# Performance work log

Hardware: AMD Instinct MI355X
Metric: run time of the kernel (lower is better)

## Reference

```python
import jax, jax.numpy as jnp
import numpy as np

EMBED_DIM = 384
NUM_HEADS = 6
HEAD_DIM = EMBED_DIM // NUM_HEADS
MLP_HIDDEN = 4 * EMBED_DIM
LN_EPS = 1e-5


def layer_norm(x, gamma, beta):
    mu = jnp.mean(x, axis=-1, keepdims=True)
    var = jnp.mean((x - mu) ** 2, axis=-1, keepdims=True)
    return (x - mu) * jax.lax.rsqrt(var + LN_EPS) * gamma + beta


def setup_inputs() -> dict:
    key = jax.random.key(0)
    ks = jax.random.split(key, 8)
    D, H = EMBED_DIM, MLP_HIDDEN
    s = 1.0 / np.sqrt(D)
    sh = 1.0 / np.sqrt(H)
    return {
        "x": jax.random.normal(ks[0], (16, 1024, D), dtype=jnp.float32),
        "ln1_g": jnp.ones((D,), jnp.float32),
        "ln1_b": jnp.zeros((D,), jnp.float32),
        "qkv_w": jax.random.uniform(ks[1], (3 * D, D), jnp.float32, -s, s),
        "qkv_b": jax.random.uniform(ks[2], (3 * D,), jnp.float32, -s, s),
        "proj_w": jax.random.uniform(ks[3], (D, D), jnp.float32, -s, s),
        "proj_b": jax.random.uniform(ks[4], (D,), jnp.float32, -s, s),
        "ln2_g": jnp.ones((D,), jnp.float32),
        "ln2_b": jnp.zeros((D,), jnp.float32),
        "fc1_w": jax.random.uniform(ks[5], (H, D), jnp.float32, -s, s),
        "fc1_b": jax.random.uniform(ks[6], (H,), jnp.float32, -s, s),
        "fc2_w": jax.random.uniform(ks[7], (D, H), jnp.float32, -sh, sh),
        "fc2_b": jnp.zeros((D,), jnp.float32),
    }


def reference(x, ln1_g, ln1_b, qkv_w, qkv_b, proj_w, proj_b,
              ln2_g, ln2_b, fc1_w, fc1_b, fc2_w, fc2_b):
    B, N, D = x.shape
    Hh, Dh = NUM_HEADS, HEAD_DIM
    scale = Dh ** -0.5

    # --- attention sublayer (pre-norm) ---
    h = layer_norm(x, ln1_g, ln1_b)
    qkv = h @ qkv_w.T + qkv_b                      # [B,N,3D]
    qkv = qkv.reshape(B, N, 3, Hh, Dh)
    q, k, v = (qkv[:, :, i].transpose(0, 2, 1, 3) for i in range(3))  # [B,H,N,Dh]
    attn = jax.nn.softmax(jnp.einsum('bhnd,bhmd->bhnm', q, k) * scale, axis=-1)
    o = jnp.einsum('bhnm,bhmd->bhnd', attn, v)     # [B,H,N,Dh]
    o = o.transpose(0, 2, 1, 3).reshape(B, N, D)
    x = x + (o @ proj_w.T + proj_b)

    # --- MLP sublayer (pre-norm) ---
    h = layer_norm(x, ln2_g, ln2_b)
    h = jax.nn.gelu(h @ fc1_w.T + fc1_b, approximate=False)
    x = x + (h @ fc2_w.T + fc2_b)
    return x
```

## Files before the change

### kernel.cpp

```cpp
#include <hip/hip_runtime.h>

typedef unsigned short u16;
typedef unsigned int   u32;
typedef __bf16  bf16x8 __attribute__((ext_vector_type(8)));
typedef __bf16  bf16x4_t __attribute__((ext_vector_type(4)));
typedef float   f32x4  __attribute__((ext_vector_type(4)));
typedef float   f32x2  __attribute__((ext_vector_type(2)));

struct Ptrs { const void* p[13]; };

extern "C" __device__ float __ocml_native_exp2_f32(float);

__device__ __forceinline__ float bf2f(u16 u) {
    union { unsigned int i; float f; } c; c.i = ((unsigned int)u) << 16; return c.f;
}
__device__ __forceinline__ u16 f2bf(float f) {
    union { float f; unsigned int i; } c; c.f = f;
    unsigned int u = c.i;
    unsigned int r = (u + 0x7fffu + ((u >> 16) & 1u)) >> 16;
    return (u16)r;
}

__device__ __forceinline__ float wave_sum(float x) {
#pragma unroll
    for (int m = 32; m >= 1; m >>= 1) x += __shfl_xor(x, m);
    return x;
}

__device__ __forceinline__ void g2l16(const u16* g, u16* l) {
    __builtin_amdgcn_global_load_lds(
        (__attribute__((address_space(1))) void*)g,
        (__attribute__((address_space(3))) void*)l, 16, 0, 0);
}

__device__ __forceinline__ int sniff_bf16(const u32* __restrict__ w) {
    int cnt = 0;
    for (int i = 0; i < 128; ++i) {
        u16 lo = (u16)(w[i] & 0xFFFFu);
        int e = (lo >> 7) & 0xFF;
        cnt += (e >= 117 && e <= 123) ? 1 : 0;
    }
    return (cnt >= 64) ? 1 : 0;
}

__global__ __launch_bounds__(256) void k_convert(Ptrs ps,
                                                 u16* __restrict__ cw,
                                                 int* __restrict__ flagp)
{
    const int cum[13] = {0,48,96,55392,55536,73968,74016,74064,74112,
                         147840,148032,221760,221808};
    const int off[12] = {0,384,768,443136,444288,591744,
                         592128,592512,592896,1182720,1184256,1774080};
    const int flag = sniff_bf16((const u32*)ps.p[3]);
    if (blockIdx.x == 0 && threadIdx.x == 0) *flagp = flag;
    int c = blockIdx.x * 256 + threadIdx.x;
    if (c >= 221808) return;
    int seg = 0;
#pragma unroll
    for (int i = 1; i < 12; ++i) seg += (c >= cum[i]) ? 1 : 0;
    int e = (c - cum[seg]) * 8;
    u16* dst = cw + off[seg] + e;
    if (flag) {
        *(uint4*)dst = *((const uint4*)ps.p[seg + 1] + (e >> 3));
    } else {
        const float* s = (const float*)ps.p[seg + 1] + e;
        u16 tmp[8];
#pragma unroll
        for (int t = 0; t < 8; ++t) tmp[t] = f2bf(s[t]);
        *(uint4*)dst = *(const uint4*)tmp;
    }
}

__global__ __launch_bounds__(256) void k_ln1cvt(const void* __restrict__ xin,
                                                const u16* __restrict__ g,
                                                const u16* __restrict__ b,
                                                u16* __restrict__ cx,
                                                u16* __restrict__ h,
                                                const int* __restrict__ flagp)
{
    const int wid = threadIdx.x >> 6, lane = threadIdx.x & 63;
    const int row = blockIdx.x * 4 + wid;
    const int e0 = lane * 6;
    float v[6]; u16 raw[6];
    if (*flagp) {
        const u16* p = (const u16*)xin + (size_t)row * 384 + e0;
        u32 w0 = *(const u32*)(p);
        u32 w1 = *(const u32*)(p + 2);
        u32 w2 = *(const u32*)(p + 4);
        raw[0] = (u16)w0; raw[1] = (u16)(w0 >> 16);
        raw[2] = (u16)w1; raw[3] = (u16)(w1 >> 16);
        raw[4] = (u16)w2; raw[5] = (u16)(w2 >> 16);
#pragma unroll
        for (int t = 0; t < 6; t++) v[t] = bf2f(raw[t]);
    } else {
        const float* p = (const float*)xin + (size_t)row * 384 + e0;
        f32x2 a0 = *(const f32x2*)(p);
        f32x2 a1 = *(const f32x2*)(p + 2);
        f32x2 a2 = *(const f32x2*)(p + 4);
        v[0] = a0[0]; v[1] = a0[1]; v[2] = a1[0];
        v[3] = a1[1]; v[4] = a2[0]; v[5] = a2[1];
#pragma unroll
        for (int t = 0; t < 6; t++) raw[t] = f2bf(v[t]);
    }
    u32* pc = (u32*)(cx + (size_t)row * 384 + e0);
    pc[0] = (u32)raw[0] | ((u32)raw[1] << 16);
    pc[1] = (u32)raw[2] | ((u32)raw[3] << 16);
    pc[2] = (u32)raw[4] | ((u32)raw[5] << 16);
    float s = 0.f;
#pragma unroll
    for (int t = 0; t < 6; t++) s += v[t];
    const float mu = wave_sum(s) * (1.0f / 384.0f);
    float vs = 0.f;
#pragma unroll
    for (int t = 0; t < 6; t++) { float d = v[t] - mu; vs += d * d; }
    const float var = wave_sum(vs) * (1.0f / 384.0f);
    const float rs = rsqrtf(var + 1e-5f);
    const u32* gg = (const u32*)(g + e0);
    const u32* bb = (const u32*)(b + e0);
    u32 gw[3] = {gg[0], gg[1], gg[2]};
    u32 bw[3] = {bb[0], bb[1], bb[2]};
    u16 ow[6];
#pragma unroll
    for (int t = 0; t < 6; t++) {
        u16 ge = (u16)(gw[t >> 1] >> ((t & 1) * 16));
        u16 be = (u16)(bw[t >> 1] >> ((t & 1) * 16));
        ow[t] = f2bf((v[t] - mu) * rs * bf2f(ge) + bf2f(be));
    }
    u32* po = (u32*)(h + (size_t)row * 384 + e0);
    po[0] = (u32)ow[0] | ((u32)ow[1] << 16);
    po[1] = (u32)ow[2] | ((u32)ow[3] << 16);
    po[2] = (u32)ow[4] | ((u32)ow[5] << 16);
}

__device__ __forceinline__ void gemm_core_128(const u16* __restrict__ A,
                                              const u16* __restrict__ B,
                                              int K, int m0, int n0,
                                              f32x4 (&acc)[4][4])
{
    __shared__ __align__(16) u16 As[128 * 64];
    __shared__ __align__(16) u16 Bs[128 * 64];

    const int tid  = threadIdx.x;
    const int lane = tid & 63;
    const int wid  = tid >> 6;
    const int wm  = (wid >> 1) * 64;
    const int wn  = (wid & 1) * 64;
    const int l15 = lane & 15;
    const int g   = lane >> 4;
    const int srow   = lane >> 3;
    const int schunk = ((lane & 7) ^ srow) * 8;

    const u16* Abase = A + (size_t)(m0 + wid * 32 + srow) * K + schunk;
    const u16* Bbase = B + (size_t)(n0 + wid * 32 + srow) * K + schunk;

    for (int kk = 0; kk < K; kk += 64) {
        __syncthreads();
#pragma unroll
        for (int t = 0; t < 4; ++t) {
            g2l16(Abase + (size_t)t * 8 * K + kk, &As[(wid * 32 + t * 8) * 64]);
            g2l16(Bbase + (size_t)t * 8 * K + kk, &Bs[(wid * 32 + t * 8) * 64]);
        }
        __syncthreads();

#pragma unroll
        for (int ks = 0; ks < 2; ++ks) {
            bf16x8 af[4], bfr[4];
#pragma unroll
            for (int i = 0; i < 4; i++) {
                int row = wm + 16 * i + l15;
                int p = ((ks * 4 + g) ^ (l15 & 7)) * 8;
                af[i] = __builtin_bit_cast(bf16x8,
                         *(const uint4*)&As[row * 64 + p]);
            }
#pragma unroll
            for (int j = 0; j < 4; j++) {
                int row = wn + 16 * j + l15;
                int p = ((ks * 4 + g) ^ (l15 & 7)) * 8;
                bfr[j] = __builtin_bit_cast(bf16x8,
                         *(const uint4*)&Bs[row * 64 + p]);
            }
#pragma unroll
            for (int i = 0; i < 4; i++)
#pragma unroll
                for (int j = 0; j < 4; j++)
                    acc[i][j] = __builtin_amdgcn_mfma_f32_16x16x32_bf16(
                                    af[i], bfr[j], acc[i][j], 0, 0, 0);
        }
    }
}

__device__ __forceinline__ void gemm_core_128x64(const u16* __restrict__ A,
                                                 const u16* __restrict__ B,
                                                 int K, int m0, int n0,
                                                 f32x4 (&acc)[4][2])
{
    __shared__ __align__(16) u16 As[128 * 64];
    __shared__ __align__(16) u16 Bs[64 * 64];

    const int tid  = threadIdx.x;
    const int lane = tid & 63;
    const int wid  = tid >> 6;
    const int wm  = (wid >> 1) * 64;
    const int wn  = (wid & 1) * 32;
    const int l15 = lane & 15;
    const int g   = lane >> 4;
    const int srow   = lane >> 3;
    const int schunk = ((lane & 7) ^ srow) * 8;

    const u16* Abase = A + (size_t)(m0 + wid * 32 + srow) * K + schunk;
    const u16* Bbase = B + (size_t)(n0 + wid * 16 + srow) * K + schunk;

    for (int kk = 0; kk < K; kk += 64) {
        __syncthreads();
#pragma unroll
        for (int t = 0; t < 4; ++t)
            g2l16(Abase + (size_t)t * 8 * K + kk, &As[(wid * 32 + t * 8) * 64]);
#pragma unroll
        for (int t = 0; t < 2; ++t)
            g2l16(Bbase + (size_t)t * 8 * K + kk, &Bs[(wid * 16 + t * 8) * 64]);
        __syncthreads();

#pragma unroll
        for (int ks = 0; ks < 2; ++ks) {
            bf16x8 af[4], bfr[2];
#pragma unroll
            for (int i = 0; i < 4; i++) {
                int row = wm + 16 * i + l15;
                int p = ((ks * 4 + g) ^ (l15 & 7)) * 8;
                af[i] = __builtin_bit_cast(bf16x8,
                         *(const uint4*)&As[row * 64 + p]);
            }
#pragma unroll
            for (int j = 0; j < 2; j++) {
                int row = wn + 16 * j + l15;
                int p = ((ks * 4 + g) ^ (l15 & 7)) * 8;
                bfr[j] = __builtin_bit_cast(bf16x8,
                         *(const uint4*)&Bs[row * 64 + p]);
            }
#pragma unroll
            for (int i = 0; i < 4; i++)
#pragma unroll
                for (int j = 0; j < 2; j++)
                    acc[i][j] = __builtin_amdgcn_mfma_f32_16x16x32_bf16(
                                    af[i], bfr[j], acc[i][j], 0, 0, 0);
        }
    }
}

__global__ __launch_bounds__(256) void k_layernorm(const u16* __restrict__ in,
                                                   const u16* __restrict__ g,
                                                   const u16* __restrict__ b,
                                                   u16* __restrict__ out,
                                                   int nrows)
{
    const int wid = threadIdx.x >> 6, lane = threadIdx.x & 63;
    const int row = blockIdx.x * 4 + wid;
    if (row >= nrows) return;
    const int e0 = lane * 6;
    float v[6];
    const u16* p = in + (size_t)row * 384 + e0;
    u32 w0 = *(const u32*)(p);
    u32 w1 = *(const u32*)(p + 2);
    u32 w2 = *(const u32*)(p + 4);
    v[0] = bf2f((u16)w0); v[1] = bf2f((u16)(w0 >> 16));
    v[2] = bf2f((u16)w1); v[3] = bf2f((u16)(w1 >> 16));
    v[4] = bf2f((u16)w2); v[5] = bf2f((u16)(w2 >> 16));
    float s = 0.f;
#pragma unroll
    for (int t = 0; t < 6; t++) s += v[t];
    const float mu = wave_sum(s) * (1.0f / 384.0f);
    float vs = 0.f;
#pragma unroll
    for (int t = 0; t < 6; t++) { float d = v[t] - mu; vs += d * d; }
    const float var = wave_sum(vs) * (1.0f / 384.0f);
    const float rs = rsqrtf(var + 1e-5f);
    const u32* gg = (const u32*)(g + e0);
    const u32* bb = (const u32*)(b + e0);
    u32 gw[3] = {gg[0], gg[1], gg[2]};
    u32 bw[3] = {bb[0], bb[1], bb[2]};
    u16 ow[6];
#pragma unroll
    for (int t = 0; t < 6; t++) {
        u16 ge = (u16)(gw[t >> 1] >> ((t & 1) * 16));
        u16 be = (u16)(bw[t >> 1] >> ((t & 1) * 16));
        ow[t] = f2bf((v[t] - mu) * rs * bf2f(ge) + bf2f(be));
    }
    u32* po = (u32*)(out + (size_t)row * 384 + e0);
    po[0] = (u32)ow[0] | ((u32)ow[1] << 16);
    po[1] = (u32)ow[2] | ((u32)ow[3] << 16);
    po[2] = (u32)ow[4] | ((u32)ow[5] << 16);
}

__global__ __launch_bounds__(256) void k_gemm_qkv(const u16* __restrict__ A,
                                                  const u16* __restrict__ W,
                                                  const u16* __restrict__ bias,
                                                  u16* __restrict__ q,
                                                  u16* __restrict__ kbuf,
                                                  u16* __restrict__ vT)
{
    const int id = blockIdx.x, slot = id & 7, idx = id >> 3;
    const int m0 = (slot * 16 + idx / 9) * 128;
    const int n0 = (idx % 9) * 128;
    f32x4 acc[4][4];
#pragma unroll
    for (int i = 0; i < 4; i++)
#pragma unroll
        for (int j = 0; j < 4; j++) acc[i][j] = f32x4{0.f, 0.f, 0.f, 0.f};
    gemm_core_128(A, W, 384, m0, n0, acc);
    const int lane = threadIdx.x & 63, wid = threadIdx.x >> 6;
    const int wm = (wid >> 1) * 64, wn = (wid & 1) * 64;
    const int l15 = lane & 15, rq = (lane >> 4) * 4;
#pragma unroll
    for (int i = 0; i < 4; i++) {
        const int grb = m0 + wm + 16 * i + rq;
        const int bb = grb >> 10, nn = grb & 1023;
#pragma unroll
        for (int j = 0; j < 4; j++) {
            const int gc = n0 + wn + 16 * j + l15;
            const int part = gc / 384, rem = gc % 384;
            const int head = rem >> 6, dh = rem & 63;
            const int bh = bb * 6 + head;
            float vals[4];
#pragma unroll
            for (int r = 0; r < 4; r++) vals[r] = acc[i][j][r] + bf2f(bias[gc]);
            if (part == 2) {
                u32 lo = (u32)f2bf(vals[0]) | ((u32)f2bf(vals[1]) << 16);
                u32 hi = (u32)f2bf(vals[2]) | ((u32)f2bf(vals[3]) << 16);
                uint2 pk; pk.x = lo; pk.y = hi;
                *(uint2*)&vT[((size_t)bh * 64 + dh) * 1024 + nn] = pk;
            } else {
                u16* dst = part ? kbuf : q;
#pragma unroll
                for (int r = 0; r < 4; r++)
                    dst[((size_t)bh * 1024 + nn + r) * 64 + dh] = f2bf(vals[r]);
            }
        }
    }
}

__global__ __launch_bounds__(256) void k_attn(const u16* __restrict__ q,
                                              const u16* __restrict__ kk,
                                              const u16* __restrict__ vT,
                                              u16* __restrict__ o)
{
    __shared__ __align__(16) u16 Ks[128 * 64];
    __shared__ __align__(16) u16 Vs[2][64 * 64];
    __shared__ __align__(16) u16 Ps[128 * 64];

    const int tid = threadIdx.x, lane = tid & 63, wid = tid >> 6;
    const int l15 = lane & 15, g = lane >> 4, q8 = g * 8;
    const int id = blockIdx.x;
    const int bh = (id & 7) * 12 + ((id >> 3) >> 3);
    const int q0 = ((id >> 3) & 7) * 128;
    const int wrow = wid * 32;

    const u16* Q = q  + (size_t)bh * 65536;
    const u16* K = kk + (size_t)bh * 65536;
    const u16* V = vT + (size_t)bh * 65536;

    const int srow   = lane >> 3;
    const int schunk = ((lane & 7) ^ srow) * 8;
    const int rd0 = ((0 + g) ^ (l15 & 7)) * 8;
    const int rd1 = ((4 + g) ^ (l15 & 7)) * 8;
    int pcol[4];
#pragma unroll
    for (int ip = 0; ip < 4; ++ip)
        pcol[ip] = (((ip * 2 + (g >> 1)) ^ (l15 & 7)) * 8) + (g & 1) * 4;

    bf16x8 aq[2][2];
#pragma unroll
    for (int jp = 0; jp < 2; ++jp)
#pragma unroll
        for (int ks = 0; ks < 2; ++ks) {
            bf16x8 t = __builtin_bit_cast(bf16x8,
                *(const uint4*)&Q[(size_t)(q0 + wrow + jp * 16 + l15) * 64
                                  + ks * 32 + q8]);
#pragma unroll
            for (int e = 0; e < 8; ++e)
                t[e] = (__bf16)((float)t[e] * 0.18033688f);
            aq[jp][ks] = t;
        }

    f32x4 ob[2][4];
#pragma unroll
    for (int i = 0; i < 2; ++i)
#pragma unroll
        for (int j = 0; j < 4; ++j) ob[i][j] = f32x4{0.f, 0.f, 0.f, 0.f};
    float lsum[2] = {0.f, 0.f};

    for (int kt2 = 0; kt2 < 8; ++kt2) {
        __syncthreads();
#pragma unroll
        for (int t = 0; t < 4; ++t) {
            int r0 = wid * 32 + t * 8;
            g2l16(&K[(size_t)(kt2 * 128 + r0 + srow) * 64 + schunk], &Ks[r0 * 64]);
        }
#pragma unroll
        for (int h = 0; h < 2; ++h)
#pragma unroll
            for (int t = 0; t < 2; ++t) {
                int r0 = wid * 16 + t * 8;
                g2l16(&V[(size_t)(r0 + srow) * 1024 + kt2 * 128 + h * 64 + schunk],
                      &Vs[h][r0 * 64]);
            }
        __syncthreads();

#pragma unroll 1
        for (int h = 0; h < 2; ++h) {
            f32x4 st[4][2];
#pragma unroll
            for (int ip = 0; ip < 4; ++ip)
#pragma unroll
                for (int jp = 0; jp < 2; ++jp) st[ip][jp] = f32x4{0.f,0.f,0.f,0.f};
            __builtin_amdgcn_s_setprio(1);
#pragma unroll
            for (int ip = 0; ip < 4; ++ip) {
                int rbase = (h * 64 + ip * 16 + l15) * 64;
                bf16x8 bk0 = __builtin_bit_cast(bf16x8,
                    *(const uint4*)&Ks[rbase + rd0]);
                bf16x8 bk1 = __builtin_bit_cast(bf16x8,
                    *(const uint4*)&Ks[rbase + rd1]);
#pragma unroll
                for (int jp = 0; jp < 2; ++jp) {
                    st[ip][jp] = __builtin_amdgcn_mfma_f32_16x16x32_bf16(
                                    bk0, aq[jp][0], st[ip][jp], 0, 0, 0);
                    st[ip][jp] = __builtin_amdgcn_mfma_f32_16x16x32_bf16(
                                    bk1, aq[jp][1], st[ip][jp], 0, 0, 0);
                }
            }
            __builtin_amdgcn_s_setprio(0);

#pragma unroll
            for (int jp = 0; jp < 2; ++jp) {
                float ps = 0.f;
#pragma unroll
                for (int ip = 0; ip < 4; ++ip)
#pragma unroll
                    for (int r = 0; r < 4; ++r) {
                        float p = __ocml_native_exp2_f32(st[ip][jp][r]);
                        st[ip][jp][r] = p;
                        ps += p;
                    }
                lsum[jp] += ps;
            }

#pragma unroll
            for (int ip = 0; ip < 4; ++ip)
#pragma unroll
                for (int jp = 0; jp < 2; ++jp) {
                    bf16x4_t pk;
#pragma unroll
                    for (int r = 0; r < 4; ++r) pk[r] = (__bf16)st[ip][jp][r];
                    *(bf16x4_t*)&Ps[(wrow + jp*16 + l15) * 64 + pcol[ip]] = pk;
                }

            __builtin_amdgcn_s_setprio(1);
#pragma unroll
            for (int ks = 0; ks < 2; ++ks) {
                const int rdo = ks ? rd1 : rd0;
                bf16x8 ap[2];
#pragma unroll
                for (int i = 0; i < 2; ++i)
                    ap[i] = __builtin_bit_cast(bf16x8,
                        *(const uint4*)&Ps[(wrow + i*16 + l15) * 64 + rdo]);
#pragma unroll
                for (int jv = 0; jv < 4; ++jv) {
                    bf16x8 bv = __builtin_bit_cast(bf16x8,
                        *(const uint4*)&Vs[h][(jv * 16 + l15) * 64 + rdo]);
#pragma unroll
                    for (int i = 0; i < 2; ++i)
                        ob[i][jv] = __builtin_amdgcn_mfma_f32_16x16x32_bf16(
                                      ap[i], bv, ob[i][jv], 0, 0, 0);
                }
            }
            __builtin_amdgcn_s_setprio(0);
        }
    }

#pragma unroll
    for (int jp = 0; jp < 2; ++jp) {
        lsum[jp] += __shfl_xor(lsum[jp], 16);
        lsum[jp] += __shfl_xor(lsum[jp], 32);
    }
    const int bb = bh / 6, hh = bh % 6;
#pragma unroll
    for (int i = 0; i < 2; ++i)
#pragma unroll
        for (int r = 0; r < 4; ++r) {
            int src = (lane & 48) | (g * 4 + r);
            float linv = 1.0f / __shfl(lsum[i], src);
            int row = q0 + wrow + i * 16 + g * 4 + r;
#pragma unroll
            for (int jv = 0; jv < 4; ++jv) {
                int dh = jv * 16 + l15;
                o[((size_t)(bb * 1024 + row)) * 384 + hh * 64 + dh] =
                    f2bf(ob[i][jv][r] * linv);
            }
        }
}

__global__ __launch_bounds__(256) void k_gemm_proj(const u16* __restrict__ A,
                                                   const u16* __restrict__ W,
                                                   const u16* __restrict__ bias,
                                                   const u16* __restrict__ xin,
                                                   u16* __restrict__ x1)
{
    const int id = blockIdx.x, slot = id & 7, idx = id >> 3;
    const int m0 = (slot * 16 + idx / 6) * 128;
    const int n0 = (idx % 6) * 64;
    f32x4 acc[4][2];
#pragma unroll
    for (int i = 0; i < 4; i++)
#pragma unroll
        for (int j = 0; j < 2; j++) acc[i][j] = f32x4{0.f, 0.f, 0.f, 0.f};
    gemm_core_128x64(A, W, 384, m0, n0, acc);
    const int lane = threadIdx.x & 63, wid = threadIdx.x >> 6;
    const int wm = (wid >> 1) * 64, wn = (wid & 1) * 32;
    const int l15 = lane & 15, rq = (lane >> 4) * 4;
#pragma unroll
    for (int i = 0; i < 4; i++)
#pragma unroll
        for (int j = 0; j < 2; j++)
#pragma unroll
            for (int r = 0; r < 4; r++) {
                int gr = m0 + wm + 16 * i + rq + r;
                int gc = n0 + wn + 16 * j + l15;
                size_t ix = (size_t)gr * 384 + gc;
                x1[ix] = f2bf(acc[i][j][r] + bf2f(bias[gc]) + bf2f(xin[ix]));
            }
}

__global__ __launch_bounds__(256) void k_gemm_fc1(const u16* __restrict__ A,
                                                  const u16* __restrict__ W,
                                                  const u16* __restrict__ bias,
                                                  u16* __restrict__ hmid)
{
    __shared__ __align__(16) u16 As[256 * 64];
    __shared__ __align__(16) u16 Bs[128 * 64];

    const int id = blockIdx.x, slot = id & 7, idx = id >> 3;
    const int m0 = (slot * 8 + idx / 12) * 256;
    const int n0 = (idx % 12) * 128;

    const int tid = threadIdx.x, lane = tid & 63, wid = tid >> 6;
    const int l15 = lane & 15, g = lane >> 4;
    const int srow = lane >> 3;
    const int schunk = ((lane & 7) ^ srow) * 8;

    const u16* Abase = A + (size_t)(m0 + wid * 64 + srow) * 384 + schunk;
    const u16* Bbase = W + (size_t)(n0 + wid * 32 + srow) * 384 + schunk;

    f32x4 acc[4][8];
#pragma unroll
    for (int i = 0; i < 4; i++)
#pragma unroll
        for (int j = 0; j < 8; j++) acc[i][j] = f32x4{0.f, 0.f, 0.f, 0.f};

    for (int kk = 0; kk < 384; kk += 64) {
        __syncthreads();
#pragma unroll
        for (int t = 0; t < 8; ++t)
            g2l16(Abase + (size_t)t * 8 * 384 + kk, &As[(wid * 64 + t * 8) * 64]);
#pragma unroll
        for (int t = 0; t < 4; ++t)
            g2l16(Bbase + (size_t)t * 8 * 384 + kk, &Bs[(wid * 32 + t * 8) * 64]);
        __syncthreads();

#pragma unroll
        for (int ks = 0; ks < 2; ++ks) {
            const int p = ((ks * 4 + g) ^ (l15 & 7)) * 8;
            bf16x8 af[4], bfr[8];
#pragma unroll
            for (int i = 0; i < 4; i++)
                af[i] = __builtin_bit_cast(bf16x8,
                    *(const uint4*)&As[(wid * 64 + 16 * i + l15) * 64 + p]);
#pragma unroll
            for (int j = 0; j < 8; j++)
                bfr[j] = __builtin_bit_cast(bf16x8,
                    *(const uint4*)&Bs[(16 * j + l15) * 64 + p]);
#pragma unroll
            for (int i = 0; i < 4; i++)
#pragma unroll
                for (int j = 0; j < 8; j++)
                    acc[i][j] = __builtin_amdgcn_mfma_f32_16x16x32_bf16(
                                    af[i], bfr[j], acc[i][j], 0, 0, 0);
        }
    }

    const int rq = g * 4;
#pragma unroll
    for (int i = 0; i < 4; i++)
#pragma unroll
        for (int j = 0; j < 8; j++)
#pragma unroll
            for (int r = 0; r < 4; r++) {
                int gr = m0 + wid * 64 + 16 * i + rq + r;
                int gc = n0 + 16 * j + l15;
                float v = acc[i][j][r] + bf2f(bias[gc]);
                float u = v * (1.5957691f + 0.0713548f * v * v);
                float ge = v * __builtin_amdgcn_rcpf(1.0f + __expf(-u));
                hmid[(size_t)gr * 1536 + gc] = f2bf(ge);
            }
}

__global__ __launch_bounds__(256) void k_gemm_fc2(const u16* __restrict__ A,
                                                  const u16* __restrict__ W,
                                                  const u16* __restrict__ bias,
                                                  const u16* __restrict__ x1,
                                                  void* __restrict__ outv,
                                                  const int* __restrict__ flagp)
{
    const int id = blockIdx.x, slot = id & 7, idx = id >> 3;
    const int m0 = (slot * 16 + idx / 6) * 128;
    const int n0 = (idx % 6) * 64;
    f32x4 acc[4][2];
#pragma unroll
    for (int i = 0; i < 4; i++)
#pragma unroll
        for (int j = 0; j < 2; j++) acc[i][j] = f32x4{0.f, 0.f, 0.f, 0.f};
    gemm_core_128x64(A, W, 1536, m0, n0, acc);
    const int lane = threadIdx.x & 63, wid = threadIdx.x >> 6;
    const int wm = (wid >> 1) * 64, wn = (wid & 1) * 32;
    const int l15 = lane & 15, rq = (lane >> 4) * 4;
    const int isbf = *flagp;
    u16*   ob = (u16*)outv;
    float* of = (float*)outv;
#pragma unroll
    for (int i = 0; i < 4; i++)
#pragma unroll
        for (int j = 0; j < 2; j++)
#pragma unroll
            for (int r = 0; r < 4; r++) {
                int gr = m0 + wm + 16 * i + rq + r;
                int gc = n0 + wn + 16 * j + l15;
                size_t ix = (size_t)gr * 384 + gc;
                float v = acc[i][j][r] + bf2f(bias[gc]) + bf2f(x1[ix]);
                if (isbf) ob[ix] = f2bf(v);
                else      of[ix] = v;
            }
}

extern "C" void kernel_launch(void* const* d_in, const int* in_sizes, int n_in,
                              void* d_out, int out_size, void* d_ws, size_t ws_size,
                              hipStream_t stream)
{
    char* ws = (char*)d_ws;
    u16*   cw   = (u16*)(ws + 0);
    int*   flag = (int*)(ws + 3548928);
    u16*   cx   = (u16*)(ws + 3549184);
    u16*   h    = (u16*)(ws + 16132096);
    u16*   x1   = (u16*)(ws + 28715008);
    u16*   q    = (u16*)(ws + 53880832);
    u16*   kbuf = (u16*)(ws + 66463744);
    u16*   vT   = (u16*)(ws + 79046656);
    u16*   o    = (u16*)(ws + 91629568);
    u16*   hmid = (u16*)(ws + 53880832);

    const u16* c_ln1_g  = cw + 0;
    const u16* c_ln1_b  = cw + 384;
    const u16* c_qkv_w  = cw + 768;
    const u16* c_qkv_b  = cw + 443136;
    const u16* c_proj_w = cw + 444288;
    const u16* c_proj_b = cw + 591744;
    const u16* c_ln2_g  = cw + 592128;
    const u16* c_ln2_b  = cw + 592512;
    const u16* c_fc1_w  = cw + 592896;
    const u16* c_fc1_b  = cw + 1182720;
    const u16* c_fc2_w  = cw + 1184256;
    const u16* c_fc2_b  = cw + 1774080;

    Ptrs ps;
    for (int i = 0; i < 13; ++i) ps.p[i] = d_in[i];

    k_convert<<<867, 256, 0, stream>>>(ps, cw, flag);
    k_ln1cvt<<<4096, 256, 0, stream>>>(d_in[0], c_ln1_g, c_ln1_b, cx, h, flag);
    k_gemm_qkv<<<1152, 256, 0, stream>>>(h, c_qkv_w, c_qkv_b, q, kbuf, vT);
    k_attn<<<768, 256, 0, stream>>>(q, kbuf, vT, o);
    k_gemm_proj<<<768, 256, 0, stream>>>(o, c_proj_w, c_proj_b, cx, x1);
    k_layernorm<<<4096, 256, 0, stream>>>(x1, c_ln2_g, c_ln2_b, h, 16384);
    k_gemm_fc1<<<768, 256, 0, stream>>>(h, c_fc1_w, c_fc1_b, hmid);
    k_gemm_fc2<<<768, 256, 0, stream>>>(hmid, c_fc2_w, c_fc2_b, x1,
                                        d_out, flag);
    (void)in_sizes; (void)n_in; (void)out_size; (void)ws_size; (void)c_fc2_b;
}
```

Measured before the change: 271.4 us.

## Split fc1 tile into two 128-row passes via shared gemm core; unroll attention head loop

```diff
diff --git a/kernel.cpp b/kernel.cpp
--- a/kernel.cpp
+++ b/kernel.cpp
@@ -405,7 +405,7 @@
             }
         __syncthreads();
 
-#pragma unroll 1
+#pragma unroll
         for (int h = 0; h < 2; ++h) {
             f32x4 st[4][2];
 #pragma unroll
@@ -535,72 +535,35 @@
                                                   const u16* __restrict__ bias,
                                                   u16* __restrict__ hmid)
 {
-    __shared__ __align__(16) u16 As[256 * 64];
-    __shared__ __align__(16) u16 Bs[128 * 64];
-
     const int id = blockIdx.x, slot = id & 7, idx = id >> 3;
-    const int m0 = (slot * 8 + idx / 12) * 256;
+    const int mbase = (slot * 8 + idx / 12) * 256;
     const int n0 = (idx % 12) * 128;
-
-    const int tid = threadIdx.x, lane = tid & 63, wid = tid >> 6;
-    const int l15 = lane & 15, g = lane >> 4;
-    const int srow = lane >> 3;
-    const int schunk = ((lane & 7) ^ srow) * 8;
-
-    const u16* Abase = A + (size_t)(m0 + wid * 64 + srow) * 384 + schunk;
-    const u16* Bbase = W + (size_t)(n0 + wid * 32 + srow) * 384 + schunk;
-
-    f32x4 acc[4][8];
-#pragma unroll
-    for (int i = 0; i < 4; i++)
-#pragma unroll
-        for (int j = 0; j < 8; j++) acc[i][j] = f32x4{0.f, 0.f, 0.f, 0.f};
-
-    for (int kk = 0; kk < 384; kk += 64) {
-        __syncthreads();
-#pragma unroll
-        for (int t = 0; t < 8; ++t)
-            g2l16(Abase + (size_t)t * 8 * 384 + kk, &As[(wid * 64 + t * 8) * 64]);
-#pragma unroll
-        for (int t = 0; t < 4; ++t)
-            g2l16(Bbase + (size_t)t * 8 * 384 + kk, &Bs[(wid * 32 + t * 8) * 64]);
-        __syncthreads();
-
-#pragma unroll
-        for (int ks = 0; ks < 2; ++ks) {
-            const int p = ((ks * 4 + g) ^ (l15 & 7)) * 8;
-            bf16x8 af[4], bfr[8];
-#pragma unroll
-            for (int i = 0; i < 4; i++)
-                af[i] = __builtin_bit_cast(bf16x8,
-                    *(const uint4*)&As[(wid * 64 + 16 * i + l15) * 64 + p]);
-#pragma unroll
-            for (int j = 0; j < 8; j++)
-                bfr[j] = __builtin_bit_cast(bf16x8,
-                    *(const uint4*)&Bs[(16 * j + l15) * 64 + p]);
-#pragma unroll
-            for (int i = 0; i < 4; i++)
-#pragma unroll
-                for (int j = 0; j < 8; j++)
-                    acc[i][j] = __builtin_amdgcn_mfma_f32_16x16x32_bf16(
-                                    af[i], bfr[j], acc[i][j], 0, 0, 0);
-        }
-    }
-
-    const int rq = g * 4;
-#pragma unroll
-    for (int i = 0; i < 4; i++)
-#pragma unroll
-        for (int j = 0; j < 8; j++)
-#pragma unroll
-            for (int r = 0; r < 4; r++) {
-                int gr = m0 + wid * 64 + 16 * i + rq + r;
-                int gc = n0 + 16 * j + l15;
-                float v = acc[i][j][r] + bf2f(bias[gc]);
-                float u = v * (1.5957691f + 0.0713548f * v * v);
-                float ge = v * __builtin_amdgcn_rcpf(1.0f + __expf(-u));
-                hmid[(size_t)gr * 1536 + gc] = f2bf(ge);
-            }
+#pragma unroll 1
+    for (int sub = 0; sub < 2; ++sub) {
+        const int m0 = mbase + sub * 128;
+        f32x4 acc[4][4];
+#pragma unroll
+        for (int i = 0; i < 4; i++)
+#pragma unroll
+            for (int j = 0; j < 4; j++) acc[i][j] = f32x4{0.f, 0.f, 0.f, 0.f};
+        gemm_core_128(A, W, 384, m0, n0, acc);
+        const int lane = threadIdx.x & 63, wid = threadIdx.x >> 6;
+        const int wm = (wid >> 1) * 64, wn = (wid & 1) * 64;
+        const int l15 = lane & 15, rq = (lane >> 4) * 4;
+#pragma unroll
+        for (int i = 0; i < 4; i++)
+#pragma unroll
+            for (int j = 0; j < 4; j++)
+#pragma unroll
+                for (int r = 0; r < 4; r++) {
+                    int gr = m0 + wm + 16 * i + rq + r;
+                    int gc = n0 + wn + 16 * j + l15;
+                    float v = acc[i][j][r] + bf2f(bias[gc]);
+                    float u = v * (1.5957691f + 0.0713548f * v * v);
+                    float ge = v * __builtin_amdgcn_rcpf(1.0f + __expf(-u));
+                    hmid[(size_t)gr * 1536 + gc] = f2bf(ge);
+                }
+    }
 }
 
 __global__ __launch_bounds__(256) void k_gemm_fc2(const u16* __restrict__ A,
```

New measurement: 280.5 us. 3.3% more time.
